# Performance work log

Hardware: AMD Instinct MI355X
Metric: run time of the kernel (lower is better)

Reference implementation:

```python
import jax, jax.numpy as jnp
import numpy as np

D_MODEL = 1024
D_HID = D_MODEL // 4
N_EXPERTS = 64
TOP_K = 2


def setup_inputs() -> dict:
    key = jax.random.key(0)
    k_x, k_w1, k_b1, k_w2, k_b2 = jax.random.split(key, 5)
    # torch Linear default init: U(-1/sqrt(fan_in), 1/sqrt(fan_in))
    s1 = 1.0 / np.sqrt(D_MODEL)
    s2 = 1.0 / np.sqrt(D_HID)
    return {
        "x": jax.random.normal(k_x, (4, 4096, D_MODEL), dtype=jnp.float32),
        "W1": jax.random.uniform(k_w1, (D_MODEL, D_HID), jnp.float32, -s1, s1),
        "b1": jax.random.uniform(k_b1, (D_HID,), jnp.float32, -s1, s1),
        "W2": jax.random.uniform(k_w2, (D_HID, N_EXPERTS), jnp.float32, -s2, s2),
        "b2": jax.random.uniform(k_b2, (N_EXPERTS,), jnp.float32, -s2, s2),
    }


def reference(x, W1, b1, W2, b2):
    # gate MLP: [B,S,D] -> [B,S,H] -> tanh -> [B,S,E]
    h = jnp.tanh(jnp.einsum("bsd,dh->bsh", x, W1) + b1)
    gate_logits = jnp.einsum("bsh,he->bse", h, W2) + b2
    # top-k selection + softmax over the k selected logits
    top_logits, top_idx = jax.lax.top_k(gate_logits, TOP_K)  # [B,S,K]
    top_gates = jax.nn.softmax(top_logits, axis=-1)          # [B,S,K]
    # scatter back into dense [B,S,E] gate tensor
    onehot = jax.nn.one_hot(top_idx, N_EXPERTS, dtype=top_gates.dtype)  # [B,S,K,E]
    gates = jnp.einsum("bsk,bske->bse", top_gates, onehot)
    return gates, gate_logits
```

## Files before the change

### kernel.cpp

```cpp
#include <hip/hip_runtime.h>
#include <math.h>


#define DM 1024
#define DH 256
#define NE 64

#define W1P_OFF 0
#define W1P_STRIDE 524288
#define W2P_OFF 1572864
#define W2P_STRIDE 32768

#define HSTR 276

typedef __attribute__((ext_vector_type(8))) short bf16x8;
typedef __attribute__((ext_vector_type(4))) float f32x4;

__device__ __forceinline__ unsigned fbits(float f) { return __float_as_uint(f); }
__device__ __forceinline__ float topf(unsigned u) { return __uint_as_float(u & 0xFFFF0000u); }

__device__ __forceinline__ void split3(float v, unsigned& h, unsigned& m, unsigned& l) {
    h = fbits(v);
    float r1 = v - topf(h);
    m = fbits(r1);
    float r2 = r1 - topf(m);
    l = fbits(r2);
}
__device__ __forceinline__ unsigned packpair(unsigned a, unsigned b) {
    return (a >> 16) | (b & 0xFFFF0000u);
}
__device__ __forceinline__ bf16x8 as_bf(uint4 u) {
    union { uint4 a; bf16x8 b; } c; c.a = u; return c.b;
}

__device__ __forceinline__ void split_pack8(float4 f0, float4 f1,
                                            bf16x8& H, bf16x8& M, bf16x8& L) {
    float v[8] = {f0.x, f0.y, f0.z, f0.w, f1.x, f1.y, f1.z, f1.w};
    unsigned hb[8], mb[8], lb[8];
#pragma unroll
    for (int j = 0; j < 8; j++) split3(v[j], hb[j], mb[j], lb[j]);
    uint4 uh = {packpair(hb[0], hb[1]), packpair(hb[2], hb[3]),
                packpair(hb[4], hb[5]), packpair(hb[6], hb[7])};
    uint4 um = {packpair(mb[0], mb[1]), packpair(mb[2], mb[3]),
                packpair(mb[4], mb[5]), packpair(mb[6], mb[7])};
    uint4 ul = {packpair(lb[0], lb[1]), packpair(lb[2], lb[3]),
                packpair(lb[4], lb[5]), packpair(lb[6], lb[7])};
    H = as_bf(uh); M = as_bf(um); L = as_bf(ul);
}


__global__ __launch_bounds__(256)
void prep_planes(const float* __restrict__ W1, const float* __restrict__ W2,
                 char* __restrict__ ws) {
    unsigned* w1p = (unsigned*)(ws + W1P_OFF);
    unsigned* w2p = (unsigned*)(ws + W2P_OFF);
    const int gt = blockIdx.x * 256 + threadIdx.x;
    if (gt < 131072) {
        const int q = gt & 3, L = (gt >> 2) & 63, nt = (gt >> 8) & 15, kc = gt >> 12;
        const int n = nt * 16 + (L & 15);
        const int k0 = kc * 32 + ((L >> 4) & 3) * 8 + 2 * q;
        float v0 = W1[(size_t)k0 * DH + n];
        float v1 = W1[(size_t)(k0 + 1) * DH + n];
        unsigned h0, m0, l0, h1, m1, l1;
        split3(v0, h0, m0, l0);
        split3(v1, h1, m1, l1);
        w1p[0 * 131072 + gt] = packpair(h0, h1);
        w1p[1 * 131072 + gt] = packpair(m0, m1);
        w1p[2 * 131072 + gt] = packpair(l0, l1);
    } else {
        const int g2 = gt - 131072;
        if (g2 < 8192) {
            const int q = g2 & 3, L = (g2 >> 2) & 63, nt = (g2 >> 8) & 3, kc = g2 >> 10;
            const int n = nt * 16 + (L & 15);
            const int k0 = kc * 32 + ((L >> 4) & 3) * 8 + 2 * q;
            float v0 = W2[k0 * NE + n];
            float v1 = W2[(k0 + 1) * NE + n];
            unsigned h0, m0, l0, h1, m1, l1;
            split3(v0, h0, m0, l0);
            split3(v1, h1, m1, l1);
            w2p[0 * 8192 + g2] = packpair(h0, h1);
            w2p[1 * 8192 + g2] = packpair(m0, m1);
            w2p[2 * 8192 + g2] = packpair(l0, l1);
        }
    }
}

__global__ __launch_bounds__(512, 2)
void fused_gating(const float* __restrict__ x, const char* __restrict__ w1p,
                  const float* __restrict__ b1, const char* __restrict__ w2p,
                  const float* __restrict__ b2, float* __restrict__ gates,
                  float* __restrict__ logits_out) {
    __shared__ __align__(16) float hlds[64 * HSTR];

    const int tid  = threadIdx.x;
    const int lane = tid & 63;
    const int wave = tid >> 6;
    const int wr = wave & 1;
    const int wc = wave >> 1;
    const int m15 = lane & 15;
    const int lq  = lane >> 4;
    const int t0 = blockIdx.x * 64;

    const float* xr0 = x + (size_t)(t0 + wr * 32 + m15) * DM + lq * 8;
    const float* xr1 = xr0 + (size_t)16 * DM;
    const char* bbase = w1p + (size_t)(wc * 4) * 1024 + lane * 16;

    f32x4 acc[2][4];
#pragma unroll
    for (int ms = 0; ms < 2; ms++)
#pragma unroll
        for (int nt = 0; nt < 4; nt++) acc[ms][nt] = (f32x4){0.f, 0.f, 0.f, 0.f};

    float4 c00 = *(const float4*)(xr0);
    float4 c01 = *(const float4*)(xr0 + 4);
    float4 c10 = *(const float4*)(xr1);
    float4 c11 = *(const float4*)(xr1 + 4);

    for (int kc = 0; kc < 32; kc++) {
        const int kn = (kc + 1) & 31;
        float4 n00 = *(const float4*)(xr0 + kn * 32);
        float4 n01 = *(const float4*)(xr0 + kn * 32 + 4);
        float4 n10 = *(const float4*)(xr1 + kn * 32);
        float4 n11 = *(const float4*)(xr1 + kn * 32 + 4);

        uint4 bfr[3][4];
#pragma unroll
        for (int p = 0; p < 3; p++)
#pragma unroll
            for (int nt = 0; nt < 4; nt++)
                bfr[p][nt] = *(const uint4*)(bbase + p * W1P_STRIDE + kc * 16384 + nt * 1024);

        bf16x8 a0h, a0m, a0l, a1h, a1m, a1l;
        split_pack8(c00, c01, a0h, a0m, a0l);
        split_pack8(c10, c11, a1h, a1m, a1l);

#pragma unroll
        for (int nt = 0; nt < 4; nt++) {
            const bf16x8 bh = as_bf(bfr[0][nt]);
            const bf16x8 bm = as_bf(bfr[1][nt]);
            const bf16x8 bl = as_bf(bfr[2][nt]);
            f32x4 a0 = acc[0][nt];
            a0 = __builtin_amdgcn_mfma_f32_16x16x32_bf16(a0h, bh, a0, 0, 0, 0);
            a0 = __builtin_amdgcn_mfma_f32_16x16x32_bf16(a0h, bm, a0, 0, 0, 0);
            a0 = __builtin_amdgcn_mfma_f32_16x16x32_bf16(a0m, bh, a0, 0, 0, 0);
            a0 = __builtin_amdgcn_mfma_f32_16x16x32_bf16(a0h, bl, a0, 0, 0, 0);
            a0 = __builtin_amdgcn_mfma_f32_16x16x32_bf16(a0l, bh, a0, 0, 0, 0);
            a0 = __builtin_amdgcn_mfma_f32_16x16x32_bf16(a0m, bm, a0, 0, 0, 0);
            acc[0][nt] = a0;
            f32x4 a1 = acc[1][nt];
            a1 = __builtin_amdgcn_mfma_f32_16x16x32_bf16(a1h, bh, a1, 0, 0, 0);
            a1 = __builtin_amdgcn_mfma_f32_16x16x32_bf16(a1h, bm, a1, 0, 0, 0);
            a1 = __builtin_amdgcn_mfma_f32_16x16x32_bf16(a1m, bh, a1, 0, 0, 0);
            a1 = __builtin_amdgcn_mfma_f32_16x16x32_bf16(a1h, bl, a1, 0, 0, 0);
            a1 = __builtin_amdgcn_mfma_f32_16x16x32_bf16(a1l, bh, a1, 0, 0, 0);
            a1 = __builtin_amdgcn_mfma_f32_16x16x32_bf16(a1m, bm, a1, 0, 0, 0);
            acc[1][nt] = a1;
        }

        c00 = n00; c01 = n01; c10 = n10; c11 = n11;
    }

#pragma unroll
    for (int nt = 0; nt < 4; nt++) {
        const int hid = wc * 64 + nt * 16 + m15;
        const float bias = b1[hid];
#pragma unroll
        for (int ms = 0; ms < 2; ms++) {
            const int tb = wr * 32 + ms * 16 + lq * 4;
#pragma unroll
            for (int r = 0; r < 4; r++)
                hlds[(tb + r) * HSTR + hid] = tanhf(acc[ms][nt][r] + bias);
        }
    }
    __syncthreads();

    if (wave < 4) {
        const float* hb = hlds + (wave * 16 + m15) * HSTR + lq * 8;
        const char* bt = w2p + lane * 16;

        f32x4 gacc[4];
#pragma unroll
        for (int nt = 0; nt < 4; nt++) gacc[nt] = (f32x4){0.f, 0.f, 0.f, 0.f};

#pragma unroll
        for (int kc = 0; kc < 8; kc++) {
            float4 f0 = *(const float4*)(hb + kc * 32);
            float4 f1 = *(const float4*)(hb + kc * 32 + 4);
            bf16x8 afh, afm, afl;
            split_pack8(f0, f1, afh, afm, afl);
#pragma unroll
            for (int nt = 0; nt < 4; nt++) {
                const char* tb = bt + (kc * 4 + nt) * 1024;
                bf16x8 bh = *(const bf16x8*)(tb + 0 * W2P_STRIDE);
                bf16x8 bm = *(const bf16x8*)(tb + 1 * W2P_STRIDE);
                bf16x8 bl = *(const bf16x8*)(tb + 2 * W2P_STRIDE);
                f32x4 a = gacc[nt];
                a = __builtin_amdgcn_mfma_f32_16x16x32_bf16(afh, bh, a, 0, 0, 0);
                a = __builtin_amdgcn_mfma_f32_16x16x32_bf16(afh, bm, a, 0, 0, 0);
                a = __builtin_amdgcn_mfma_f32_16x16x32_bf16(afm, bh, a, 0, 0, 0);
                a = __builtin_amdgcn_mfma_f32_16x16x32_bf16(afh, bl, a, 0, 0, 0);
                a = __builtin_amdgcn_mfma_f32_16x16x32_bf16(afl, bh, a, 0, 0, 0);
                a = __builtin_amdgcn_mfma_f32_16x16x32_bf16(afm, bm, a, 0, 0, 0);
                gacc[nt] = a;
            }
        }

        float b2v[4];
#pragma unroll
        for (int nt = 0; nt < 4; nt++) b2v[nt] = b2[nt * 16 + m15];

#pragma unroll
        for (int r = 0; r < 4; r++) {
            float v[4]; int e[4];
#pragma unroll
            for (int nt = 0; nt < 4; nt++) { v[nt] = gacc[nt][r] + b2v[nt]; e[nt] = nt * 16 + m15; }

            float a1 = v[0], a2 = v[1]; int j1 = e[0], j2 = e[1];
            if (v[1] > v[0]) { a1 = v[1]; j1 = e[1]; a2 = v[0]; j2 = e[0]; }
#pragma unroll
            for (int t = 2; t < 4; t++) {
                if (v[t] > a1) { a2 = a1; j2 = j1; a1 = v[t]; j1 = e[t]; }
                else if (v[t] > a2) { a2 = v[t]; j2 = e[t]; }
            }
#pragma unroll
            for (int off = 1; off < 16; off <<= 1) {
                float ob1 = __shfl_xor(a1, off, 64); int oj1 = __shfl_xor(j1, off, 64);
                float ob2 = __shfl_xor(a2, off, 64); int oj2 = __shfl_xor(j2, off, 64);
                bool bw = (ob1 > a1) || (ob1 == a1 && oj1 < j1);
                float w1v = bw ? ob1 : a1; int w1i = bw ? oj1 : j1;
                float lv = bw ? a1 : ob1;  int li  = bw ? j1 : oj1;
                float rv = bw ? ob2 : a2;  int ri  = bw ? oj2 : j2;
                bool cw = (lv > rv) || (lv == rv && li < ri);
                a1 = w1v; j1 = w1i;
                a2 = cw ? lv : rv; j2 = cw ? li : ri;
            }
            float ex = __expf(a2 - a1);
            float inv = 1.f / (1.f + ex);
            float g1 = inv, g2 = ex * inv;

            const size_t row = (size_t)(t0 + wave * 16 + lq * 4 + r) * NE;
#pragma unroll
            for (int nt = 0; nt < 4; nt++) {
                float gv = (e[nt] == j1) ? g1 : ((e[nt] == j2) ? g2 : 0.f);
                gates[row + e[nt]] = gv;
                logits_out[row + e[nt]] = v[nt];
            }
        }
    }
}

extern "C" void kernel_launch(void* const* d_in, const int* in_sizes, int n_in,
                              void* d_out, int out_size, void* d_ws, size_t ws_size,
                              hipStream_t stream) {
    const float* x  = (const float*)d_in[0];
    const float* W1 = (const float*)d_in[1];
    const float* b1 = (const float*)d_in[2];
    const float* W2 = (const float*)d_in[3];
    const float* b2 = (const float*)d_in[4];

    const int T = in_sizes[0] / DM;
    char* ws = (char*)d_ws;
    float* gates  = (float*)d_out;
    float* logits = (float*)d_out + (size_t)T * NE;

    prep_planes<<<(131072 + 8192) / 256, 256, 0, stream>>>(W1, W2, ws);
    fused_gating<<<T / 64, 512, 0, stream>>>(x, ws + W1P_OFF, b1, ws + W2P_OFF, b2,
                                             gates, logits);
}
```

Before: 167.5 us.

## Shrink token tile to 32 and prefetch W1 planes instead of x

```diff
diff --git a/kernel.cpp b/kernel.cpp
--- a/kernel.cpp
+++ b/kernel.cpp
@@ -85,60 +85,61 @@
     }
 }
 
-__global__ __launch_bounds__(512, 2)
+__global__ __launch_bounds__(512, 4)
 void fused_gating(const float* __restrict__ x, const char* __restrict__ w1p,
                   const float* __restrict__ b1, const char* __restrict__ w2p,
                   const float* __restrict__ b2, float* __restrict__ gates,
                   float* __restrict__ logits_out) {
-    __shared__ __align__(16) float hlds[64 * HSTR];
+    __shared__ __align__(16) float hlds[32 * HSTR];
 
     const int tid  = threadIdx.x;
     const int lane = tid & 63;
     const int wave = tid >> 6;
-    const int wr = wave & 1;
-    const int wc = wave >> 1;
     const int m15 = lane & 15;
     const int lq  = lane >> 4;
-    const int t0 = blockIdx.x * 64;
-
-    const float* xr0 = x + (size_t)(t0 + wr * 32 + m15) * DM + lq * 8;
+    const int t0 = blockIdx.x * 32;
+
+    const float* xr0 = x + (size_t)(t0 + m15) * DM + lq * 8;
     const float* xr1 = xr0 + (size_t)16 * DM;
-    const char* bbase = w1p + (size_t)(wc * 4) * 1024 + lane * 16;
-
-    f32x4 acc[2][4];
+    const char* bbase = w1p + (size_t)(wave * 2) * 1024 + lane * 16;
+
+    f32x4 acc[2][2];
 #pragma unroll
     for (int ms = 0; ms < 2; ms++)
 #pragma unroll
-        for (int nt = 0; nt < 4; nt++) acc[ms][nt] = (f32x4){0.f, 0.f, 0.f, 0.f};
-
-    float4 c00 = *(const float4*)(xr0);
-    float4 c01 = *(const float4*)(xr0 + 4);
-    float4 c10 = *(const float4*)(xr1);
-    float4 c11 = *(const float4*)(xr1 + 4);
-
+        for (int nt = 0; nt < 2; nt++) acc[ms][nt] = (f32x4){0.f, 0.f, 0.f, 0.f};
+
+    uint4 bc[3][2];
+#pragma unroll
+    for (int p = 0; p < 3; p++)
+#pragma unroll
+        for (int nt = 0; nt < 2; nt++)
+            bc[p][nt] = *(const uint4*)(bbase + p * W1P_STRIDE + nt * 1024);
+
+#pragma unroll 2
     for (int kc = 0; kc < 32; kc++) {
+        float4 c00 = *(const float4*)(xr0 + kc * 32);
+        float4 c01 = *(const float4*)(xr0 + kc * 32 + 4);
+        float4 c10 = *(const float4*)(xr1 + kc * 32);
+        float4 c11 = *(const float4*)(xr1 + kc * 32 + 4);
+
         const int kn = (kc + 1) & 31;
-        float4 n00 = *(const float4*)(xr0 + kn * 32);
-        float4 n01 = *(const float4*)(xr0 + kn * 32 + 4);
-        float4 n10 = *(const float4*)(xr1 + kn * 32);
-        float4 n11 = *(const float4*)(xr1 + kn * 32 + 4);
-
-        uint4 bfr[3][4];
+        uint4 bn[3][2];
 #pragma unroll
         for (int p = 0; p < 3; p++)
 #pragma unroll
-            for (int nt = 0; nt < 4; nt++)
-                bfr[p][nt] = *(const uint4*)(bbase + p * W1P_STRIDE + kc * 16384 + nt * 1024);
+            for (int nt = 0; nt < 2; nt++)
+                bn[p][nt] = *(const uint4*)(bbase + p * W1P_STRIDE + kn * 16384 + nt * 1024);
 
         bf16x8 a0h, a0m, a0l, a1h, a1m, a1l;
         split_pack8(c00, c01, a0h, a0m, a0l);
         split_pack8(c10, c11, a1h, a1m, a1l);
 
 #pragma unroll
-        for (int nt = 0; nt < 4; nt++) {
-            const bf16x8 bh = as_bf(bfr[0][nt]);
-            const bf16x8 bm = as_bf(bfr[1][nt]);
-            const bf16x8 bl = as_bf(bfr[2][nt]);
+        for (int nt = 0; nt < 2; nt++) {
+            const bf16x8 bh = as_bf(bc[0][nt]);
+            const bf16x8 bm = as_bf(bc[1][nt]);
+            const bf16x8 bl = as_bf(bc[2][nt]);
             f32x4 a0 = acc[0][nt];
             a0 = __builtin_amdgcn_mfma_f32_16x16x32_bf16(a0h, bh, a0, 0, 0, 0);
             a0 = __builtin_amdgcn_mfma_f32_16x16x32_bf16(a0h, bm, a0, 0, 0, 0);
@@ -157,16 +158,19 @@
             acc[1][nt] = a1;
         }
 
-        c00 = n00; c01 = n01; c10 = n10; c11 = n11;
-    }
-
-#pragma unroll
-    for (int nt = 0; nt < 4; nt++) {
-        const int hid = wc * 64 + nt * 16 + m15;
+#pragma unroll
+        for (int p = 0; p < 3; p++)
+#pragma unroll
+            for (int nt = 0; nt < 2; nt++) bc[p][nt] = bn[p][nt];
+    }
+
+#pragma unroll
+    for (int nt = 0; nt < 2; nt++) {
+        const int hid = wave * 32 + nt * 16 + m15;
         const float bias = b1[hid];
 #pragma unroll
         for (int ms = 0; ms < 2; ms++) {
-            const int tb = wr * 32 + ms * 16 + lq * 4;
+            const int tb = ms * 16 + lq * 4;
 #pragma unroll
             for (int r = 0; r < 4; r++)
                 hlds[(tb + r) * HSTR + hid] = tanhf(acc[ms][nt][r] + bias);
@@ -174,7 +178,7 @@
     }
     __syncthreads();
 
-    if (wave < 4) {
+    if (wave < 2) {
         const float* hb = hlds + (wave * 16 + m15) * HSTR + lq * 8;
         const char* bt = w2p + lane * 16;
 
@@ -264,6 +268,6 @@
     float* logits = (float*)d_out + (size_t)T * NE;
 
     prep_planes<<<(131072 + 8192) / 256, 256, 0, stream>>>(W1, W2, ws);
-    fused_gating<<<T / 64, 512, 0, stream>>>(x, ws + W1P_OFF, b1, ws + W2P_OFF, b2,
+    fused_gating<<<T / 32, 512, 0, stream>>>(x, ws + W1P_OFF, b1, ws + W2P_OFF, b2,
                                              gates, logits);
 }
```

Measured after the change: 186.0 us. 11.1% more time.
